# Performance work log

Measured on AMD Instinct MI355X. Metric: run time of the kernel, lower is better.

## Reference

```python
import jax, jax.numpy as jnp
import numpy as np

N, C, D, H, O = 8192, 100, 128, 128, 64


def setup_inputs() -> dict:
    key = jax.random.key(0)
    k1, k2, k3, k4 = jax.random.split(key, 4)
    x = jax.random.normal(k1, (N, D), dtype=jnp.float32)
    cat_ids = jax.random.randint(k2, (N,), 0, C)
    W1 = 0.02 * jax.random.normal(k3, (C, D, H), dtype=jnp.float32)
    b1 = jnp.zeros((C, H), dtype=jnp.float32)
    W2 = 0.02 * jax.random.normal(k4, (C, H, O), dtype=jnp.float32)
    b2 = jnp.zeros((C, O), dtype=jnp.float32)
    return {"x": x, "cat_ids": cat_ids, "W1": W1, "b1": b1, "W2": W2, "b2": b2}


def reference(x, cat_ids, W1, b1, W2, b2):
    # Layer 1: per-token category-weight gather + matmul + bias, then ReLU.
    # selected_W1: [N, D, H] (the large gathered intermediate, as in the torch code)
    h = jax.nn.relu(jnp.einsum('nd,ndh->nh', x, W1[cat_ids]) + b1[cat_ids])
    # Layer 2: [N, H] x [N, H, O] -> [N, O]
    out = jnp.einsum('nh,nho->no', h, W2[cat_ids]) + b2[cat_ids]
    return out
```

## Files before the change

kernel.cpp:

```cpp
#include <hip/hip_runtime.h>


#define N_TOK 8192
#define C_CAT 100
#define D_IN  128
#define H_MID 128
#define O_OUT 64
#define TPB   64
#define MAX_ITEMS (C_CAT + N_TOK / TPB)

typedef __attribute__((ext_vector_type(8))) short short8;
typedef __attribute__((ext_vector_type(4))) float floatx4;

__global__ __launch_bounds__(1024) void prologue_kernel(
    const int* __restrict__ cat_ids, int* __restrict__ ws) {
  __shared__ int cnt[C_CAT];
  __shared__ int cur[C_CAT];
  __shared__ int sc[128], sk[128];
  int t = threadIdx.x;
  if (t < C_CAT) cnt[t] = 0;
  __syncthreads();

  int ids[8];
  #pragma unroll
  for (int k = 0; k < 8; ++k) {
    ids[k] = cat_ids[t + (k << 10)];
    atomicAdd(&cnt[ids[k]], 1);
  }
  __syncthreads();

  int v = 0, ck = 0;
  if (t < 128) {
    v  = (t < C_CAT) ? cnt[t] : 0;
    ck = (v + TPB - 1) / TPB;
    sc[t] = v; sk[t] = ck;
  }
  __syncthreads();
  for (int off = 1; off < 128; off <<= 1) {
    int a = 0, b = 0;
    if (t < 128 && t >= off) { a = sc[t - off]; b = sk[t - off]; }
    __syncthreads();
    if (t < 128) { sc[t] += a; sk[t] += b; }
    __syncthreads();
  }
  if (t < C_CAT) {
    int start = sc[t] - v;
    int ibase = sk[t] - ck;
    cur[t] = start;
    int* items = ws + 272;
    for (int k = 0; k < ck; ++k) {
      items[3 * (ibase + k) + 0] = t;
      items[3 * (ibase + k) + 1] = start + k * TPB;
      items[3 * (ibase + k) + 2] = min(TPB, v - k * TPB);
    }
  }
  if (t == 127) ws[256] = sk[127];
  __syncthreads();

  #pragma unroll
  for (int k = 0; k < 8; ++k) {
    int pos = atomicAdd(&cur[ids[k]], 1);
    ws[2048 + pos] = t + (k << 10);
  }
}

__device__ __forceinline__ void bf16_split(float f, short& hi, short& lo) {
  unsigned b  = __builtin_bit_cast(unsigned, f);
  unsigned hb = b & 0xFFFF0000u;
  hi = (short)(hb >> 16);
  float r = f - __builtin_bit_cast(float, hb);
  unsigned rb = __builtin_bit_cast(unsigned, r);
  lo = (short)((rb + 0x7FFFu + ((rb >> 16) & 1u)) >> 16);
}

__global__ __launch_bounds__(256) void mlp_kernel(
    const float* __restrict__ x,  const float* __restrict__ W1,
    const float* __restrict__ b1, const float* __restrict__ W2,
    const float* __restrict__ b2, float* __restrict__ out,
    const int* __restrict__ ws) {
  int bid = blockIdx.x;
  if (bid >= ws[256]) return;
  const int* item = ws + 272 + 3 * bid;
  int cat = item[0], start = item[1], cnt = item[2];
  const int* sorted = ws + 2048;

  __shared__ __align__(16) short XF[2][8192];
  __shared__ __align__(16) short WF[2][8192];
  __shared__ int toks[TPB];

  int tid  = threadIdx.x;
  int lane = tid & 63;
  int wv   = tid >> 6;

  if (tid < TPB) toks[tid] = (tid < cnt) ? sorted[start + tid] : sorted[start];
  __syncthreads();

  #pragma unroll
  for (int p = 0; p < 4; ++p) {
    int f = ((tid + (p << 8)) >> 6);
    int L = lane;
    int mt = f & 3, ks = f >> 2;
    int m  = (mt << 4) + (L & 15);
    int k0 = (ks << 5) + ((L >> 4) << 3);
    const float* xr = x + (size_t)toks[m] * D_IN + k0;
    float4 v0 = *(const float4*)(xr);
    float4 v1 = *(const float4*)(xr + 4);
    float xv[8] = {v0.x, v0.y, v0.z, v0.w, v1.x, v1.y, v1.z, v1.w};
    short8 h8, l8;
    #pragma unroll
    for (int j = 0; j < 8; ++j) { short hh, ll; bf16_split(xv[j], hh, ll); h8[j] = hh; l8[j] = ll; }
    ((short8*)XF[0])[(f << 6) + L] = h8;
    ((short8*)XF[1])[(f << 6) + L] = l8;
  }

  floatx4 acc[4][2];
  #pragma unroll
  for (int mt = 0; mt < 4; ++mt)
    #pragma unroll
    for (int ntl = 0; ntl < 2; ++ntl) acc[mt][ntl] = 0.f;

  for (int ph = 0; ph < 2; ++ph) {
    #pragma unroll
    for (int p = 0; p < 4; ++p) {
      int f = ((tid + (p << 8)) >> 6);
      int L = lane;
      int nt = f & 7, ksl = f >> 3;
      int n  = (nt << 4) + (L & 15);
      int kb = (ph << 6) + (ksl << 5) + ((L >> 4) << 3);
      const float* wsrc = W1 + ((size_t)cat * D_IN + kb) * H_MID + n;
      float wv8[8];
      #pragma unroll
      for (int j = 0; j < 8; ++j) wv8[j] = wsrc[(size_t)j * H_MID];
      short8 h8, l8;
      #pragma unroll
      for (int j = 0; j < 8; ++j) { short hh, ll; bf16_split(wv8[j], hh, ll); h8[j] = hh; l8[j] = ll; }
      ((short8*)WF[0])[(f << 6) + L] = h8;
      ((short8*)WF[1])[(f << 6) + L] = l8;
    }
    __syncthreads();

    #pragma unroll
    for (int ksl = 0; ksl < 2; ++ksl) {
      int ksg = (ph << 1) + ksl;
      short8 ah[4], al[4];
      #pragma unroll
      for (int mt = 0; mt < 4; ++mt) {
        ah[mt] = ((short8*)XF[0])[(((ksg << 2) + mt) << 6) + lane];
        al[mt] = ((short8*)XF[1])[(((ksg << 2) + mt) << 6) + lane];
      }
      short8 bh[2], bl[2];
      #pragma unroll
      for (int ntl = 0; ntl < 2; ++ntl) {
        int f = (ksl << 3) + (wv << 1) + ntl;
        bh[ntl] = ((short8*)WF[0])[(f << 6) + lane];
        bl[ntl] = ((short8*)WF[1])[(f << 6) + lane];
      }
      #pragma unroll
      for (int mt = 0; mt < 4; ++mt)
        #pragma unroll
        for (int ntl = 0; ntl < 2; ++ntl) {
          acc[mt][ntl] = __builtin_amdgcn_mfma_f32_16x16x32_bf16(ah[mt], bh[ntl], acc[mt][ntl], 0, 0, 0);
          acc[mt][ntl] = __builtin_amdgcn_mfma_f32_16x16x32_bf16(ah[mt], bl[ntl], acc[mt][ntl], 0, 0, 0);
          acc[mt][ntl] = __builtin_amdgcn_mfma_f32_16x16x32_bf16(al[mt], bh[ntl], acc[mt][ntl], 0, 0, 0);
        }
    }
    __syncthreads();
  }

  #pragma unroll
  for (int ntl = 0; ntl < 2; ++ntl) {
    int n = (wv << 5) + (ntl << 4) + (lane & 15);
    float b1v = b1[(size_t)cat * H_MID + n];
    #pragma unroll
    for (int mt = 0; mt < 4; ++mt) {
      #pragma unroll
      for (int r = 0; r < 4; ++r) {
        float hfull = fmaxf(acc[mt][ntl][r] + b1v, 0.f);
        short hh, hl; bf16_split(hfull, hh, hl);
        int m  = (mt << 4) + ((lane >> 4) << 2) + r;
        int L2 = (((n >> 3) & 3) << 4) + (m & 15);
        int sa = (((wv << 2) + mt) << 9) + (L2 << 3) + (n & 7);
        XF[0][sa] = hh; XF[1][sa] = hl;
      }
    }
  }

  #pragma unroll
  for (int p = 0; p < 4; ++p) {
    int f = ((tid + (p << 8)) >> 6);
    int L = lane;
    int nt = f & 3, ks = f >> 2;
    int n  = (nt << 4) + (L & 15);
    int kb = (ks << 5) + ((L >> 4) << 3);
    const float* wsrc = W2 + ((size_t)cat * H_MID + kb) * O_OUT + n;
    float wv8[8];
    #pragma unroll
    for (int j = 0; j < 8; ++j) wv8[j] = wsrc[(size_t)j * O_OUT];
    short8 h8, l8;
    #pragma unroll
    for (int j = 0; j < 8; ++j) { short hh, ll; bf16_split(wv8[j], hh, ll); h8[j] = hh; l8[j] = ll; }
    ((short8*)WF[0])[(f << 6) + L] = h8;
    ((short8*)WF[1])[(f << 6) + L] = l8;
  }
  __syncthreads();

  floatx4 acc2[4];
  #pragma unroll
  for (int mt = 0; mt < 4; ++mt) acc2[mt] = 0.f;

  #pragma unroll
  for (int ks = 0; ks < 4; ++ks) {
    short8 bh = ((short8*)WF[0])[(((ks << 2) + wv) << 6) + lane];
    short8 bl = ((short8*)WF[1])[(((ks << 2) + wv) << 6) + lane];
    #pragma unroll
    for (int mt = 0; mt < 4; ++mt) {
      short8 ah = ((short8*)XF[0])[(((ks << 2) + mt) << 6) + lane];
      short8 al = ((short8*)XF[1])[(((ks << 2) + mt) << 6) + lane];
      acc2[mt] = __builtin_amdgcn_mfma_f32_16x16x32_bf16(ah, bh, acc2[mt], 0, 0, 0);
      acc2[mt] = __builtin_amdgcn_mfma_f32_16x16x32_bf16(ah, bl, acc2[mt], 0, 0, 0);
      acc2[mt] = __builtin_amdgcn_mfma_f32_16x16x32_bf16(al, bh, acc2[mt], 0, 0, 0);
    }
  }

  {
    int n2 = (wv << 4) + (lane & 15);
    float b2v = b2[(size_t)cat * O_OUT + n2];
    #pragma unroll
    for (int mt = 0; mt < 4; ++mt) {
      #pragma unroll
      for (int r = 0; r < 4; ++r) {
        int m = (mt << 4) + ((lane >> 4) << 2) + r;
        if (m < cnt)
          out[(size_t)toks[m] * O_OUT + n2] = acc2[mt][r] + b2v;
      }
    }
  }
}

extern "C" void kernel_launch(void* const* d_in, const int* in_sizes, int n_in,
                              void* d_out, int out_size, void* d_ws, size_t ws_size,
                              hipStream_t stream) {
  const float* x       = (const float*)d_in[0];
  const int*   cat_ids = (const int*)  d_in[1];
  const float* W1      = (const float*)d_in[2];
  const float* b1      = (const float*)d_in[3];
  const float* W2      = (const float*)d_in[4];
  const float* b2      = (const float*)d_in[5];
  float* out = (float*)d_out;
  int*   ws  = (int*)d_ws;

  prologue_kernel<<<1, 1024, 0, stream>>>(cat_ids, ws);
  mlp_kernel<<<MAX_ITEMS, 256, 0, stream>>>(x, W1, b1, W2, b2, out, ws);
}
```

Measured before the change: 89.48 us.

## Split prologue into multi-block histogram/scan/scatter and preload weights into registers

The single-block prologue is replaced by four kernels (zero, multi-block histogram, scan, multi-block scatter) so the token sort runs in parallel across blocks. The MLP kernel now issues every global load of x, W1, W2 and the biases up front into registers, removes the shared weight buffer and its barriers, and splits weights to bf16 hi/lo in registers right before each MFMA. The aim is to hide load latency and remove the serial prologue. The cost is three extra kernel launches and much higher register pressure, capped at one block per SIMD group via launch bounds.

Result: no change. 89.44 us (-0.0%).

```diff
diff --git a/kernel.cpp b/kernel.cpp
--- a/kernel.cpp
+++ b/kernel.cpp
@@ -9,44 +9,44 @@
 #define TPB   64
 #define MAX_ITEMS (C_CAT + N_TOK / TPB)
 
+
 typedef __attribute__((ext_vector_type(8))) short short8;
 typedef __attribute__((ext_vector_type(4))) float floatx4;
 
-__global__ __launch_bounds__(1024) void prologue_kernel(
+__global__ __launch_bounds__(256) void zero_kernel(int* __restrict__ ws) {
+  ws[threadIdx.x] = 0;
+}
+
+__global__ __launch_bounds__(256) void hist_kernel(
     const int* __restrict__ cat_ids, int* __restrict__ ws) {
-  __shared__ int cnt[C_CAT];
-  __shared__ int cur[C_CAT];
+  __shared__ int h[C_CAT];
+  int t = threadIdx.x;
+  if (t < C_CAT) h[t] = 0;
+  __syncthreads();
+  int g = blockIdx.x * 256 + t;
+  atomicAdd(&h[cat_ids[g]], 1);
+  __syncthreads();
+  if (t < C_CAT && h[t] > 0) atomicAdd(&ws[t], h[t]);
+}
+
+__global__ __launch_bounds__(128) void scan_kernel(int* __restrict__ ws) {
   __shared__ int sc[128], sk[128];
   int t = threadIdx.x;
-  if (t < C_CAT) cnt[t] = 0;
-  __syncthreads();
-
-  int ids[8];
-  #pragma unroll
-  for (int k = 0; k < 8; ++k) {
-    ids[k] = cat_ids[t + (k << 10)];
-    atomicAdd(&cnt[ids[k]], 1);
-  }
-  __syncthreads();
-
-  int v = 0, ck = 0;
-  if (t < 128) {
-    v  = (t < C_CAT) ? cnt[t] : 0;
-    ck = (v + TPB - 1) / TPB;
-    sc[t] = v; sk[t] = ck;
-  }
+  int v  = (t < C_CAT) ? ws[t] : 0;
+  int ck = (v + TPB - 1) / TPB;
+  sc[t] = v; sk[t] = ck;
   __syncthreads();
   for (int off = 1; off < 128; off <<= 1) {
     int a = 0, b = 0;
-    if (t < 128 && t >= off) { a = sc[t - off]; b = sk[t - off]; }
+    if (t >= off) { a = sc[t - off]; b = sk[t - off]; }
     __syncthreads();
-    if (t < 128) { sc[t] += a; sk[t] += b; }
+    sc[t] += a; sk[t] += b;
     __syncthreads();
   }
   if (t < C_CAT) {
     int start = sc[t] - v;
     int ibase = sk[t] - ck;
-    cur[t] = start;
+    ws[128 + t] = start;
     int* items = ws + 272;
     for (int k = 0; k < ck; ++k) {
       items[3 * (ibase + k) + 0] = t;
@@ -55,13 +55,22 @@
     }
   }
   if (t == 127) ws[256] = sk[127];
-  __syncthreads();
-
-  #pragma unroll
-  for (int k = 0; k < 8; ++k) {
-    int pos = atomicAdd(&cur[ids[k]], 1);
-    ws[2048 + pos] = t + (k << 10);
-  }
+}
+
+__global__ __launch_bounds__(256) void scatter_kernel(
+    const int* __restrict__ cat_ids, int* __restrict__ ws) {
+  __shared__ int lcnt[C_CAT];
+  __shared__ int gbase[C_CAT];
+  int t = threadIdx.x;
+  if (t < C_CAT) lcnt[t] = 0;
+  __syncthreads();
+  int g = blockIdx.x * 256 + t;
+  int c = cat_ids[g];
+  int r = atomicAdd(&lcnt[c], 1);
+  __syncthreads();
+  if (t < C_CAT && lcnt[t] > 0) gbase[t] = atomicAdd(&ws[128 + t], lcnt[t]);
+  __syncthreads();
+  ws[2048 + gbase[c] + r] = g;
 }
 
 __device__ __forceinline__ void bf16_split(float f, short& hi, short& lo) {
@@ -73,7 +82,12 @@
   lo = (short)((rb + 0x7FFFu + ((rb >> 16) & 1u)) >> 16);
 }
 
-__global__ __launch_bounds__(256) void mlp_kernel(
+__device__ __forceinline__ void split8(const float* v, short8& h8, short8& l8) {
+  #pragma unroll
+  for (int j = 0; j < 8; ++j) { short hh, ll; bf16_split(v[j], hh, ll); h8[j] = hh; l8[j] = ll; }
+}
+
+__global__ __launch_bounds__(256, 1) void mlp_kernel(
     const float* __restrict__ x,  const float* __restrict__ W1,
     const float* __restrict__ b1, const float* __restrict__ W2,
     const float* __restrict__ b2, float* __restrict__ out,
@@ -85,33 +99,70 @@
   const int* sorted = ws + 2048;
 
   __shared__ __align__(16) short XF[2][8192];
-  __shared__ __align__(16) short WF[2][8192];
   __shared__ int toks[TPB];
 
   int tid  = threadIdx.x;
   int lane = tid & 63;
   int wv   = tid >> 6;
 
-  if (tid < TPB) toks[tid] = (tid < cnt) ? sorted[start + tid] : sorted[start];
-  __syncthreads();
-
+  if (tid < TPB) toks[tid] = sorted[start + min(tid, cnt - 1)];
+
+  int mrow = (wv << 4) + (lane & 15);
+  int tok  = sorted[start + (mrow < cnt ? mrow : 0)];
+  const float* xr = x + (size_t)tok * D_IN + ((lane >> 4) << 3);
+  float xq[4][8];
   #pragma unroll
   for (int p = 0; p < 4; ++p) {
-    int f = ((tid + (p << 8)) >> 6);
-    int L = lane;
-    int mt = f & 3, ks = f >> 2;
-    int m  = (mt << 4) + (L & 15);
-    int k0 = (ks << 5) + ((L >> 4) << 3);
-    const float* xr = x + (size_t)toks[m] * D_IN + k0;
-    float4 v0 = *(const float4*)(xr);
-    float4 v1 = *(const float4*)(xr + 4);
-    float xv[8] = {v0.x, v0.y, v0.z, v0.w, v1.x, v1.y, v1.z, v1.w};
+    *(float4*)&xq[p][0] = *(const float4*)(xr + (p << 5));
+    *(float4*)&xq[p][4] = *(const float4*)(xr + (p << 5) + 4);
+  }
+
+  const float* W1c = W1 + (size_t)cat * (D_IN * H_MID);
+  float w1a[4][8], w1b[4][8];
+  #pragma unroll
+  for (int p = 0; p < 4; ++p) {
+    int f   = (p << 2) + wv;
+    int nt  = f & 7;
+    int ksl = f >> 3;
+    int n   = (nt << 4) + (lane & 15);
+    int kb  = (ksl << 5) + ((lane >> 4) << 3);
+    #pragma unroll
+    for (int j = 0; j < 8; ++j) {
+      w1a[p][j] = W1c[(size_t)(kb + j) * H_MID + n];
+      w1b[p][j] = W1c[(size_t)(64 + kb + j) * H_MID + n];
+    }
+  }
+
+  const float* W2c = W2 + (size_t)cat * (H_MID * O_OUT);
+  float w2r[4][8];
+  {
+    int n = (wv << 4) + (lane & 15);
+    #pragma unroll
+    for (int p = 0; p < 4; ++p) {
+      int kb = (p << 5) + ((lane >> 4) << 3);
+      #pragma unroll
+      for (int j = 0; j < 8; ++j)
+        w2r[p][j] = W2c[(size_t)(kb + j) * O_OUT + n];
+    }
+  }
+
+  float b1v[2];
+  #pragma unroll
+  for (int ntl = 0; ntl < 2; ++ntl) {
+    int ntile = wv + (ntl << 2);
+    b1v[ntl] = b1[(size_t)cat * H_MID + (ntile << 4) + (lane & 15)];
+  }
+  float b2v = b2[(size_t)cat * O_OUT + (wv << 4) + (lane & 15)];
+
+  #pragma unroll
+  for (int p = 0; p < 4; ++p) {
     short8 h8, l8;
-    #pragma unroll
-    for (int j = 0; j < 8; ++j) { short hh, ll; bf16_split(xv[j], hh, ll); h8[j] = hh; l8[j] = ll; }
-    ((short8*)XF[0])[(f << 6) + L] = h8;
-    ((short8*)XF[1])[(f << 6) + L] = l8;
-  }
+    split8(xq[p], h8, l8);
+    int f = (p << 2) + wv;
+    ((short8*)XF[0])[(f << 6) + lane] = h8;
+    ((short8*)XF[1])[(f << 6) + lane] = l8;
+  }
+  __syncthreads();
 
   floatx4 acc[4][2];
   #pragma unroll
@@ -119,89 +170,50 @@
     #pragma unroll
     for (int ntl = 0; ntl < 2; ++ntl) acc[mt][ntl] = 0.f;
 
-  for (int ph = 0; ph < 2; ++ph) {
-    #pragma unroll
-    for (int p = 0; p < 4; ++p) {
-      int f = ((tid + (p << 8)) >> 6);
-      int L = lane;
-      int nt = f & 7, ksl = f >> 3;
-      int n  = (nt << 4) + (L & 15);
-      int kb = (ph << 6) + (ksl << 5) + ((L >> 4) << 3);
-      const float* wsrc = W1 + ((size_t)cat * D_IN + kb) * H_MID + n;
-      float wv8[8];
-      #pragma unroll
-      for (int j = 0; j < 8; ++j) wv8[j] = wsrc[(size_t)j * H_MID];
-      short8 h8, l8;
-      #pragma unroll
-      for (int j = 0; j < 8; ++j) { short hh, ll; bf16_split(wv8[j], hh, ll); h8[j] = hh; l8[j] = ll; }
-      ((short8*)WF[0])[(f << 6) + L] = h8;
-      ((short8*)WF[1])[(f << 6) + L] = l8;
-    }
-    __syncthreads();
-
-    #pragma unroll
-    for (int ksl = 0; ksl < 2; ++ksl) {
-      int ksg = (ph << 1) + ksl;
-      short8 ah[4], al[4];
-      #pragma unroll
-      for (int mt = 0; mt < 4; ++mt) {
-        ah[mt] = ((short8*)XF[0])[(((ksg << 2) + mt) << 6) + lane];
-        al[mt] = ((short8*)XF[1])[(((ksg << 2) + mt) << 6) + lane];
+  #pragma unroll
+  for (int ksg = 0; ksg < 4; ++ksg) {
+    short8 ah[4], al[4];
+    #pragma unroll
+    for (int mt = 0; mt < 4; ++mt) {
+      ah[mt] = ((short8*)XF[0])[(((ksg << 2) + mt) << 6) + lane];
+      al[mt] = ((short8*)XF[1])[(((ksg << 2) + mt) << 6) + lane];
+    }
+    short8 bh[2], bl[2];
+    #pragma unroll
+    for (int ntl = 0; ntl < 2; ++ntl) {
+      const float* wreg = (ksg < 2) ? w1a[((ksg & 1) << 1) + ntl]
+                                    : w1b[((ksg & 1) << 1) + ntl];
+      split8(wreg, bh[ntl], bl[ntl]);
+    }
+    #pragma unroll
+    for (int mt = 0; mt < 4; ++mt)
+      #pragma unroll
+      for (int ntl = 0; ntl < 2; ++ntl) {
+        acc[mt][ntl] = __builtin_amdgcn_mfma_f32_16x16x32_bf16(ah[mt], bh[ntl], acc[mt][ntl], 0, 0, 0);
+        acc[mt][ntl] = __builtin_amdgcn_mfma_f32_16x16x32_bf16(ah[mt], bl[ntl], acc[mt][ntl], 0, 0, 0);
+        acc[mt][ntl] = __builtin_amdgcn_mfma_f32_16x16x32_bf16(al[mt], bh[ntl], acc[mt][ntl], 0, 0, 0);
       }
-      short8 bh[2], bl[2];
-      #pragma unroll
-      for (int ntl = 0; ntl < 2; ++ntl) {
-        int f = (ksl << 3) + (wv << 1) + ntl;
-        bh[ntl] = ((short8*)WF[0])[(f << 6) + lane];
-        bl[ntl] = ((short8*)WF[1])[(f << 6) + lane];
-      }
-      #pragma unroll
-      for (int mt = 0; mt < 4; ++mt)
-        #pragma unroll
-        for (int ntl = 0; ntl < 2; ++ntl) {
-          acc[mt][ntl] = __builtin_amdgcn_mfma_f32_16x16x32_bf16(ah[mt], bh[ntl], acc[mt][ntl], 0, 0, 0);
-          acc[mt][ntl] = __builtin_amdgcn_mfma_f32_16x16x32_bf16(ah[mt], bl[ntl], acc[mt][ntl], 0, 0, 0);
-          acc[mt][ntl] = __builtin_amdgcn_mfma_f32_16x16x32_bf16(al[mt], bh[ntl], acc[mt][ntl], 0, 0, 0);
-        }
-    }
-    __syncthreads();
-  }
+  }
+  __syncthreads();
 
   #pragma unroll
   for (int ntl = 0; ntl < 2; ++ntl) {
-    int n = (wv << 5) + (ntl << 4) + (lane & 15);
-    float b1v = b1[(size_t)cat * H_MID + n];
+    int ntile = wv + (ntl << 2);
+    int n = (ntile << 4) + (lane & 15);
     #pragma unroll
     for (int mt = 0; mt < 4; ++mt) {
       #pragma unroll
       for (int r = 0; r < 4; ++r) {
-        float hfull = fmaxf(acc[mt][ntl][r] + b1v, 0.f);
+        float hfull = fmaxf(acc[mt][ntl][r] + b1v[ntl], 0.f);
         short hh, hl; bf16_split(hfull, hh, hl);
         int m  = (mt << 4) + ((lane >> 4) << 2) + r;
+        int f2 = ((n >> 5) << 2) + mt;
         int L2 = (((n >> 3) & 3) << 4) + (m & 15);
-        int sa = (((wv << 2) + mt) << 9) + (L2 << 3) + (n & 7);
+        int sa = (f2 << 9) + (L2 << 3) + (n & 7);
         XF[0][sa] = hh; XF[1][sa] = hl;
       }
     }
   }
-
-  #pragma unroll
-  for (int p = 0; p < 4; ++p) {
-    int f = ((tid + (p << 8)) >> 6);
-    int L = lane;
-    int nt = f & 3, ks = f >> 2;
-    int n  = (nt << 4) + (L & 15);
-    int kb = (ks << 5) + ((L >> 4) << 3);
-    const float* wsrc = W2 + ((size_t)cat * H_MID + kb) * O_OUT + n;
-    float wv8[8];
-    #pragma unroll
-    for (int j = 0; j < 8; ++j) wv8[j] = wsrc[(size_t)j * O_OUT];
-    short8 h8, l8;
-    #pragma unroll
-    for (int j = 0; j < 8; ++j) { short hh, ll; bf16_split(wv8[j], hh, ll); h8[j] = hh; l8[j] = ll; }
-    ((short8*)WF[0])[(f << 6) + L] = h8;
-    ((short8*)WF[1])[(f << 6) + L] = l8;
-  }
   __syncthreads();
 
   floatx4 acc2[4];
@@ -210,8 +222,8 @@
 
   #pragma unroll
   for (int ks = 0; ks < 4; ++ks) {
-    short8 bh = ((short8*)WF[0])[(((ks << 2) + wv) << 6) + lane];
-    short8 bl = ((short8*)WF[1])[(((ks << 2) + wv) << 6) + lane];
+    short8 bh, bl;
+    split8(w2r[ks], bh, bl);
     #pragma unroll
     for (int mt = 0; mt < 4; ++mt) {
       short8 ah = ((short8*)XF[0])[(((ks << 2) + mt) << 6) + lane];
@@ -224,7 +236,6 @@
 
   {
     int n2 = (wv << 4) + (lane & 15);
-    float b2v = b2[(size_t)cat * O_OUT + n2];
     #pragma unroll
     for (int mt = 0; mt < 4; ++mt) {
       #pragma unroll
@@ -249,6 +260,9 @@
   float* out = (float*)d_out;
   int*   ws  = (int*)d_ws;
 
-  prologue_kernel<<<1, 1024, 0, stream>>>(cat_ids, ws);
-  mlp_kernel<<<MAX_ITEMS, 256, 0, stream>>>(x, W1, b1, W2, b2, out, ws);
-}
+  zero_kernel   <<<1,            256, 0, stream>>>(ws);
+  hist_kernel   <<<N_TOK / 256,  256, 0, stream>>>(cat_ids, ws);
+  scan_kernel   <<<1,            128, 0, stream>>>(ws);
+  scatter_kernel<<<N_TOK / 256,  256, 0, stream>>>(cat_ids, ws);
+  mlp_kernel    <<<MAX_ITEMS,    256, 0, stream>>>(x, W1, b1, W2, b2, out, ws);
+}
```
